# Optimization experiments

Hardware: AMD Instinct MI355X
Metric: run time of the kernel (lower is better)

## Reference

```python
import jax, jax.numpy as jnp
import numpy as np

DIM = 192
HEADS = 6
HIDDEN = 384  # int(dim * mlp_ratio)


def conv2d(x, w, b=None, padding=0, groups=1):
    out = jax.lax.conv_general_dilated(
        x, w, (1, 1), [(padding, padding), (padding, padding)],
        feature_group_count=groups,
        dimension_numbers=('NCHW', 'OIHW', 'NCHW'))
    return out if b is None else out + b[None, :, None, None]


def layernorm(x, g, b, eps=1e-5):
    m = x.mean(-1, keepdims=True)
    v = x.var(-1, keepdims=True)  # biased, matches torch LayerNorm
    return (x - m) / jnp.sqrt(v + eps) * g + b


def l2norm(x, eps=1e-12):  # F.normalize(dim=-1)
    n = jnp.linalg.norm(x, axis=-1, keepdims=True)
    return x / jnp.maximum(n, eps)


def setup_inputs() -> dict:
    key = jax.random.key(0)
    ks = jax.random.split(key, 12)
    s = 0.02
    return {
        'x': jax.random.normal(ks[0], (4, DIM, 128, 128), dtype=jnp.float32),
        'g1': jnp.ones((DIM,), jnp.float32),
        'b1': jnp.zeros((DIM,), jnp.float32),
        'w_qkv': jax.random.normal(ks[1], (3 * DIM, DIM, 1, 1), jnp.float32) * s,
        'w_dw': jax.random.normal(ks[2], (3 * DIM, 1, 3, 3), jnp.float32) * s,
        'temp': jnp.ones((HEADS, 1, 1), jnp.float32),
        'w_head': jax.random.normal(ks[3], (HEADS, HEADS, 3, 3), jnp.float32) * s,
        'w_proj': jax.random.normal(ks[4], (DIM, DIM, 1, 1), jnp.float32) * s,
        'g2': jnp.ones((DIM,), jnp.float32),
        'b2': jnp.zeros((DIM,), jnp.float32),
        'w_fc1': jax.random.normal(ks[5], (HIDDEN, DIM), jnp.float32) * s,
        'b_fc1': jnp.zeros((HIDDEN,), jnp.float32),
        'w_fc2': jax.random.normal(ks[6], (DIM, HIDDEN), jnp.float32) * s,
        'b_fc2': jnp.zeros((DIM,), jnp.float32),
        'w_sa': jax.random.normal(ks[7], (1, DIM, 3, 3), jnp.float32) * s,
        'b_sa': jnp.zeros((1,), jnp.float32),
    }


def reference(x, g1, b1, w_qkv, w_dw, temp, w_head, w_proj, g2, b2,
              w_fc1, b_fc1, w_fc2, b_fc2, w_sa, b_sa):
    b, c, h, w = x.shape
    hw = h * w
    # norm1 (note: original code re-assigns x, so residual uses normed x)
    xf = x.reshape(b, c, hw).transpose(0, 2, 1)          # [b, hw, c]
    x1 = layernorm(xf, g1, b1).transpose(0, 2, 1).reshape(b, c, h, w)
    # channel attention (Restormer style)
    qkv = conv2d(conv2d(x1, w_qkv), w_dw, padding=1, groups=3 * c)
    q, k, v = jnp.split(qkv, 3, axis=1)
    cp = c // HEADS
    q = l2norm(q.reshape(b, HEADS, cp, hw))
    k = l2norm(k.reshape(b, HEADS, cp, hw))
    v = v.reshape(b, HEADS, cp, hw)
    attn = jnp.einsum('bhcn,bhdn->bhcd', q, k) * temp    # [b, heads, cp, cp]
    attn = conv2d(attn, w_head, padding=1)               # conv over head channels
    attn = jax.nn.softmax(attn, axis=-1)
    out = jnp.einsum('bhcd,bhdn->bhcn', attn, v).reshape(b, c, h, w)
    out = conv2d(out, w_proj)
    x2 = x1 + out
    # MLP branch with spatial-gating attn
    x3 = x2.reshape(b, c, hw).transpose(0, 2, 1)         # [b, hw, c]
    y = layernorm(x3, g2, b2)
    y = jax.nn.gelu(y @ w_fc1.T + b_fc1, approximate=False)
    y = y @ w_fc2.T + b_fc2
    y = jax.nn.gelu(y, approximate=False)                # SAAttn act_fn
    y4 = y.reshape(b, h, w, c).transpose(0, 3, 1, 2)     # [b, c, h, w]
    gate = jax.nn.sigmoid(conv2d(y4, w_sa, b_sa, padding=1))  # [b,1,h,w]
    y = (y4 * gate).reshape(b, c, hw).transpose(0, 2, 1)
    x4 = x3 + y
    return x4.transpose(0, 2, 1).reshape(b, c, h, w)
```

## Files before the change

### kernel.cpp

```cpp
#include <hip/hip_runtime.h>
#include <hip/hip_bf16.h>
#include <math.h>

using bf16 = __hip_bfloat16;

static constexpr int CDIM   = 192;
static constexpr int HEADS  = 6;
static constexpr int CP     = 32;
static constexpr int HIDDEN = 384;
static constexpr int HImg   = 128;
static constexpr int WImg   = 128;
static constexpr int HW     = HImg * WImg;
static constexpr int BATCH  = 4;
static constexpr int PCHUNK = 256;
static constexpr int CSPLIT = 12;
static constexpr int DWCHUNK = 4;

typedef __attribute__((ext_vector_type(8))) short short8;
typedef __attribute__((ext_vector_type(4))) float f32x4;
typedef __attribute__((ext_vector_type(4))) unsigned short ushort4v;
typedef __attribute__((ext_vector_type(8))) unsigned short ushort8v;

template<typename T> __device__ inline float tof(T v);
template<> __device__ inline float tof<float>(float v){ return v; }
template<> __device__ inline float tof<bf16>(bf16 v){ return __bfloat162float(v); }

template<typename T> __device__ inline T fromf(float v);
template<> __device__ inline float fromf<float>(float v){ return v; }
template<> __device__ inline bf16  fromf<bf16>(float v){ return __float2bfloat16(v); }

__device__ inline unsigned short f2bf_bits(float f){
    bf16 h = __float2bfloat16(f);
    return *reinterpret_cast<unsigned short*>(&h);
}
__device__ inline float bfbits2f(unsigned short u){
    union { unsigned int i; float f; } c; c.i = ((unsigned int)u) << 16; return c.f;
}

__device__ inline float gelu_exact(float x){
    return 0.5f * x * (1.0f + erff(x * 0.70710678118654752440f));
}

__device__ inline void load4f(const float* p, float* f){
    f32x4 v = *reinterpret_cast<const f32x4*>(p);
    f[0]=v[0]; f[1]=v[1]; f[2]=v[2]; f[3]=v[3];
}
__device__ inline void load4f(const bf16* p, float* f){
    ushort4v v = *reinterpret_cast<const ushort4v*>(p);
    f[0]=bfbits2f(v[0]); f[1]=bfbits2f(v[1]); f[2]=bfbits2f(v[2]); f[3]=bfbits2f(v[3]);
}

__device__ __forceinline__ void gload16(const bf16* g, bf16* l){
    __builtin_amdgcn_global_load_lds(
        (const __attribute__((address_space(1))) void*)g,
        (__attribute__((address_space(3))) void*)l, 16, 0, 0);
}

__global__ __launch_bounds__(256) void convw_kernel(
    const float* __restrict__ w_qkv, const float* __restrict__ w_proj,
    const float* __restrict__ w_fc1, const float* __restrict__ w_fc2,
    bf16* __restrict__ wq, bf16* __restrict__ wp,
    bf16* __restrict__ wf1, bf16* __restrict__ wf2)
{
    int i = blockIdx.x * 256 + threadIdx.x;
    const int n0 = 576*192, n1 = n0 + 192*192, n2 = n1 + 384*192, n3 = n2 + 192*384;
    if (i < n0)      wq[i]       = fromf<bf16>(w_qkv[i]);
    else if (i < n1) wp[i - n0]  = fromf<bf16>(w_proj[i - n0]);
    else if (i < n2) wf1[i - n1] = fromf<bf16>(w_fc1[i - n1]);
    else if (i < n3) wf2[i - n2] = fromf<bf16>(w_fc2[i - n2]);
}

template<typename T, bool WRES>
__global__ __launch_bounds__(256) void ln_fused_kernel(
    const T* __restrict__ in, const float* __restrict__ g,
    const float* __restrict__ b, bf16* __restrict__ resF, bf16* __restrict__ outT)
{
    int z = blockIdx.y, p0 = blockIdx.x * 64;
    __shared__ float tile[CDIM][65];
    __shared__ float sred[4][64], s2red[4][64];
    __shared__ float mrow[64], rrow[64];
    const T* ib = in + (size_t)z * CDIM * HW + p0;
    int tid = threadIdx.x;
    for (int j = tid; j < CDIM * 16; j += 256){
        int c = j >> 4, p4 = (j & 15) * 4;
        float f[4];
        load4f(ib + (size_t)c * HW + p4, f);
        tile[c][p4]   = f[0]; tile[c][p4+1] = f[1];
        tile[c][p4+2] = f[2]; tile[c][p4+3] = f[3];
    }
    __syncthreads();
    int p = tid & 63, q = tid >> 6;
    float s = 0.f, s2 = 0.f;
    #pragma unroll 4
    for (int c = q * 48; c < q * 48 + 48; ++c){
        float v = tile[c][p]; s += v; s2 += v * v;
    }
    sred[q][p] = s; s2red[q][p] = s2;
    __syncthreads();
    if (tid < 64){
        float ts = sred[0][tid] + sred[1][tid] + sred[2][tid] + sred[3][tid];
        float t2 = s2red[0][tid] + s2red[1][tid] + s2red[2][tid] + s2red[3][tid];
        float mean = ts * (1.0f / CDIM);
        float var  = t2 * (1.0f / CDIM) - mean * mean;
        mrow[tid] = mean;
        rrow[tid] = rsqrtf(var + 1e-5f);
    }
    __syncthreads();
    unsigned short* oT = (unsigned short*)(outT + ((size_t)z * HW + p0) * CDIM);
    for (int j = tid; j < 64 * 48; j += 256){
        int pr = j / 48, c4 = (j % 48) * 4;
        float m = mrow[pr], r = rrow[pr];
        ushort4v o;
        #pragma unroll
        for (int k = 0; k < 4; ++k){
            int c = c4 + k;
            o[k] = f2bf_bits((tile[c][pr] - m) * r * g[c] + b[c]);
        }
        *(ushort4v*)&oT[(size_t)pr * CDIM + c4] = o;
    }
    if (WRES){
        unsigned short* oF = (unsigned short*)resF + (size_t)z * CDIM * HW + p0;
        for (int j = tid; j < CDIM * 16; j += 256){
            int c = j >> 4, p4 = (j & 15) * 4;
            float gg = g[c], bb = b[c];
            ushort4v v;
            #pragma unroll
            for (int k = 0; k < 4; ++k)
                v[k] = f2bf_bits((tile[c][p4 + k] - mrow[p4 + k]) * rrow[p4 + k] * gg + bb);
            *(ushort4v*)&oF[(size_t)c * HW + p4] = v;
        }
    }
}

template<int EPI>
__global__ __launch_bounds__(256) void gemm_mfma_kernel(
    const bf16* __restrict__ Wb, const bf16* __restrict__ XT,
    void* __restrict__ Cout, const float* __restrict__ bias,
    const bf16* __restrict__ res, int M, int K)
{
    __shared__ bf16 smem[24576];
    int z  = blockIdx.z;
    int n0 = blockIdx.x * 128;
    int m0 = blockIdx.y * 64;
    const bf16* Xb = XT + (size_t)z * (size_t)HW * K;
    int tid  = threadIdx.x;
    int lane = tid & 63, wid = tid >> 6;
    int wm = wid & 1, wn = wid >> 1;
    int r16 = lane & 15, grp = lane >> 4;

    f32x4 acc[2][4];
    #pragma unroll
    for (int i = 0; i < 2; ++i)
        #pragma unroll
        for (int j = 0; j < 4; ++j){ f32x4 zz = {0.f,0.f,0.f,0.f}; acc[i][j] = zz; }

    auto STAGE = [&](int kt, int buf){
        bf16* Al = smem + buf * 12288;
        bf16* Bl = Al + 4096;
        #pragma unroll
        for (int i = 0; i < 2; ++i){
            int s = i * 256 + tid;
            int row = s >> 3, ch = s & 7;
            gload16(Wb + (size_t)(m0 + row) * K + kt * 64 + ((ch ^ (row & 7)) * 8),
                    Al + s * 8);
        }
        #pragma unroll
        for (int i = 0; i < 4; ++i){
            int s = i * 256 + tid;
            int row = s >> 3, ch = s & 7;
            gload16(Xb + (size_t)(n0 + row) * K + kt * 64 + ((ch ^ (row & 7)) * 8),
                    Bl + s * 8);
        }
    };

    int nkt = K >> 6;
    STAGE(0, 0);
    int cur = 0;
    for (int kt = 0; kt < nkt; ++kt){
        if (kt + 1 < nkt){
            STAGE(kt + 1, cur ^ 1);
            asm volatile("s_waitcnt vmcnt(6)" ::: "memory");
        } else {
            asm volatile("s_waitcnt vmcnt(0)" ::: "memory");
        }
        __builtin_amdgcn_s_barrier();
        bf16* Al = smem + cur * 12288;
        bf16* Bl = Al + 4096;
        #pragma unroll
        for (int ks = 0; ks < 2; ++ks){
            int kel = ks * 32 + grp * 8;
            short8 a[2], b[4];
            #pragma unroll
            for (int fi = 0; fi < 2; ++fi){
                int row = wm * 32 + fi * 16 + r16;
                a[fi] = *reinterpret_cast<const short8*>(Al + row * 64 + (kel ^ ((row & 7) * 8)));
            }
            #pragma unroll
            for (int fj = 0; fj < 4; ++fj){
                int row = wn * 64 + fj * 16 + r16;
                b[fj] = *reinterpret_cast<const short8*>(Bl + row * 64 + (kel ^ ((row & 7) * 8)));
            }
            #pragma unroll
            for (int fi = 0; fi < 2; ++fi)
                #pragma unroll
                for (int fj = 0; fj < 4; ++fj)
                    acc[fi][fj] = __builtin_amdgcn_mfma_f32_16x16x32_bf16(
                        a[fi], b[fj], acc[fi][fj], 0, 0, 0);
        }
        asm volatile("s_waitcnt lgkmcnt(0)" ::: "memory");
        __builtin_amdgcn_sched_barrier(0);
        __builtin_amdgcn_s_barrier();
        cur ^= 1;
    }

    if (EPI == 3){
        unsigned short* T = (unsigned short*)smem;
        #pragma unroll
        for (int fi = 0; fi < 2; ++fi)
            #pragma unroll
            for (int fj = 0; fj < 4; ++fj){
                int nl = wn * 64 + fj * 16 + r16;
                int mb = wm * 32 + fi * 16 + grp * 4;
                #pragma unroll
                for (int rr = 0; rr < 4; ++rr){
                    float v = gelu_exact(acc[fi][fj][rr] + bias[m0 + mb + rr]);
                    T[nl * 72 + mb + rr] = f2bf_bits(v);
                }
            }
        __syncthreads();
        bf16* Y = (bf16*)Cout;
        int rrow = tid >> 1, half = tid & 1;
        const short8* srcv = reinterpret_cast<const short8*>(T + rrow * 72 + half * 32);
        short8* dstv = reinterpret_cast<short8*>(
            Y + ((size_t)z * HW + n0 + rrow) * M + m0 + half * 32);
        #pragma unroll
        for (int i = 0; i < 4; ++i) dstv[i] = srcv[i];
        return;
    }

    {
        unsigned short* T = (unsigned short*)smem;
        #pragma unroll
        for (int fi = 0; fi < 2; ++fi)
            #pragma unroll
            for (int fj = 0; fj < 4; ++fj){
                int m = wm * 32 + fi * 16 + grp * 4;
                int n = wn * 64 + fj * 16 + r16;
                #pragma unroll
                for (int rr = 0; rr < 4; ++rr)
                    T[(m + rr) * 136 + n] = f2bf_bits(acc[fi][fj][rr]);
            }
        __syncthreads();
        int row = tid >> 2, c8 = (tid & 3) * 8;
        bf16* Cb = (bf16*)Cout;
        size_t gbase = (size_t)z * M * HW + (size_t)(m0 + row) * HW + n0 + c8;
        float bv = (EPI == 2) ? bias[m0 + row] : 0.f;
        #pragma unroll
        for (int j = 0; j < 4; ++j){
            int coff = j * 32;
            ushort8v t8 = *(const ushort8v*)&T[row * 136 + c8 + coff];
            ushort8v o8;
            if (EPI == 0){
                o8 = t8;
            } else if (EPI == 1){
                ushort8v r8 = *(const ushort8v*)((const unsigned short*)res + gbase + coff);
                #pragma unroll
                for (int k = 0; k < 8; ++k)
                    o8[k] = f2bf_bits(bfbits2f(t8[k]) + bfbits2f(r8[k]));
            } else {
                #pragma unroll
                for (int k = 0; k < 8; ++k)
                    o8[k] = f2bf_bits(gelu_exact(bfbits2f(t8[k]) + bv));
            }
            *(ushort8v*)((unsigned short*)Cb + gbase + coff) = o8;
        }
    }
}

__global__ __launch_bounds__(256) void dw_kernel(
    const bf16* __restrict__ in, const float* __restrict__ wdw,
    bf16* __restrict__ out, float* __restrict__ sqp)
{
    int ch = blockIdx.y, z = blockIdx.z;
    int tid = threadIdx.x;
    int rp = tid >> 4;
    int xx = (tid & 15) * 8;
    int y0 = blockIdx.x * 32 + rp * 2;
    const unsigned short* p =
        (const unsigned short*)(in + ((size_t)z * 3 * CDIM + ch) * HW);
    float w[9];
    #pragma unroll
    for (int t = 0; t < 9; ++t) w[t] = wdw[ch * 9 + t];
    float f[4][8], lf[4], rf[4];
    #pragma unroll
    for (int r = 0; r < 4; ++r){
        int iy = y0 - 1 + r;
        if (iy >= 0 && iy < HImg){
            ushort8v v8 = *(const ushort8v*)(p + iy * WImg + xx);
            #pragma unroll
            for (int j = 0; j < 8; ++j) f[r][j] = bfbits2f(v8[j]);
        } else {
            #pragma unroll
            for (int j = 0; j < 8; ++j) f[r][j] = 0.f;
        }
        float l = __shfl_up(f[r][7], 1);
        float rr_ = __shfl_down(f[r][0], 1);
        lf[r] = (xx == 0) ? 0.f : l;
        rf[r] = (xx + 8 >= WImg) ? 0.f : rr_;
    }
    float sq = 0.f;
    unsigned short* ob = (unsigned short*)(out + ((size_t)z * 3 * CDIM + ch) * HW);
    #pragma unroll
    for (int orow = 0; orow < 2; ++orow){
        ushort8v o8;
        #pragma unroll
        for (int j = 0; j < 8; ++j){
            float a = 0.f;
            #pragma unroll
            for (int dy = 0; dy < 3; ++dy){
                int r = orow + dy;
                float e0 = (j == 0) ? lf[r] : f[r][j - 1];
                float e2 = (j == 7) ? rf[r] : f[r][j + 1];
                a = fmaf(w[dy*3], e0, fmaf(w[dy*3+1], f[r][j], fmaf(w[dy*3+2], e2, a)));
            }
            o8[j] = f2bf_bits(a);
            sq = fmaf(a, a, sq);
        }
        *(ushort8v*)(ob + (y0 + orow) * WImg + xx) = o8;
    }
    if (ch < 2 * CDIM){
        #pragma unroll
        for (int m = 1; m < 64; m <<= 1) sq += __shfl_xor(sq, m, 64);
        __shared__ float red[4];
        if ((tid & 63) == 0) red[tid >> 6] = sq;
        __syncthreads();
        if (tid == 0)
            sqp[((size_t)ch * BATCH + z) * DWCHUNK + blockIdx.x] =
                red[0] + red[1] + red[2] + red[3];
    }
}

__global__ __launch_bounds__(256) void attn_qk_kernel(
    const bf16* __restrict__ qkv, const float* __restrict__ sqp,
    const float* __restrict__ temp, float* __restrict__ part)
{
    int chunk = blockIdx.x;
    int h = blockIdx.y, z = blockIdx.z;
    __shared__ unsigned short qs[CP][PCHUNK + 4];
    __shared__ unsigned short ks[CP][PCHUNK + 4];
    __shared__ float invqs[CP], invks[CP];
    int tid = threadIdx.x;
    if (tid < 2 * CP){
        int which = tid >> 5, cc = tid & 31;
        int ch = which * CDIM + h * CP + cc;
        const float* sp = &sqp[((size_t)ch * BATCH + z) * DWCHUNK];
        float s = sp[0] + sp[1] + sp[2] + sp[3];
        float inv = 1.0f / fmaxf(sqrtf(s), 1e-12f);
        (which ? invks : invqs)[cc] = inv;
    }
    int n0 = chunk * PCHUNK;
    const unsigned short* qb = (const unsigned short*)(qkv + ((size_t)z * 3 * CDIM + h * CP) * HW);
    const unsigned short* kb = (const unsigned short*)(qkv + ((size_t)z * 3 * CDIM + CDIM + h * CP) * HW);
    for (int i = tid; i < CP * (PCHUNK / 4); i += 256){
        int r = i >> 6, p4 = i & 63;
        *(ushort4v*)&qs[r][p4 * 4] = *(const ushort4v*)&qb[(size_t)r * HW + n0 + p4 * 4];
        *(ushort4v*)&ks[r][p4 * 4] = *(const ushort4v*)&kb[(size_t)r * HW + n0 + p4 * 4];
    }
    __syncthreads();
    int c  = tid >> 3;
    int d0 = (tid & 7) * 4;
    float acc[4] = {0.f, 0.f, 0.f, 0.f};
    for (int p4 = 0; p4 < PCHUNK / 4; ++p4){
        ushort4v qv = *(const ushort4v*)&qs[c][p4 * 4];
        float qf0 = bfbits2f(qv[0]), qf1 = bfbits2f(qv[1]);
        float qf2 = bfbits2f(qv[2]), qf3 = bfbits2f(qv[3]);
        #pragma unroll
        for (int j = 0; j < 4; ++j){
            ushort4v kv = *(const ushort4v*)&ks[d0 + j][p4 * 4];
            acc[j] = fmaf(qf0, bfbits2f(kv[0]),
                     fmaf(qf1, bfbits2f(kv[1]),
                     fmaf(qf2, bfbits2f(kv[2]),
                     fmaf(qf3, bfbits2f(kv[3]), acc[j]))));
        }
    }
    float sc = invqs[c] * temp[h];
    size_t base = ((size_t)chunk * BATCH * HEADS + (size_t)z * HEADS + h) * CP * CP
                + c * CP + d0;
    #pragma unroll
    for (int j = 0; j < 4; ++j)
        part[base + j] = acc[j] * sc * invks[d0 + j];
}

__global__ __launch_bounds__(256) void attn_reduce_kernel(
    const float* __restrict__ part, float* __restrict__ attn)
{
    int idx = blockIdx.x * 256 + threadIdx.x;
    float s = 0.f;
    for (int ch = 0; ch < HW / PCHUNK; ++ch)
        s += part[(size_t)ch * (BATCH * HEADS * CP * CP) + idx];
    attn[idx] = s;
}

__global__ __launch_bounds__(256) void headconv_softmax_kernel(
    const float* __restrict__ attn, const float* __restrict__ wh,
    float* __restrict__ attn2)
{
    int oh = blockIdx.x, z = blockIdx.y;
    __shared__ float wsm[HEADS * 9];
    __shared__ float ain[HEADS][CP * CP];
    __shared__ float aout[CP * CP];
    int tid = threadIdx.x;
    if (tid < HEADS * 9) wsm[tid] = wh[oh * HEADS * 9 + tid];
    for (int i = tid; i < HEADS * CP * CP; i += 256)
        ain[i >> 10][i & 1023] = attn[((size_t)z * HEADS + (i >> 10)) * CP * CP + (i & 1023)];
    __syncthreads();
    for (int idx = tid; idx < CP * CP; idx += 256){
        int i = idx >> 5, j = idx & 31;
        float acc = 0.f;
        #pragma unroll
        for (int ih = 0; ih < HEADS; ++ih){
            #pragma unroll
            for (int dy = 0; dy < 3; ++dy){
                int ii = i + dy - 1;
                if (ii < 0 || ii >= CP) continue;
                #pragma unroll
                for (int dx = 0; dx < 3; ++dx){
                    int jj = j + dx - 1;
                    if (jj < 0 || jj >= CP) continue;
                    acc += wsm[ih * 9 + dy * 3 + dx] * ain[ih][ii * CP + jj];
                }
            }
        }
        aout[idx] = acc;
    }
    __syncthreads();
    int r = tid >> 3, l8 = tid & 7;
    float v[4];
    #pragma unroll
    for (int k = 0; k < 4; ++k) v[k] = aout[r * CP + l8 * 4 + k];
    float mx = fmaxf(fmaxf(v[0], v[1]), fmaxf(v[2], v[3]));
    #pragma unroll
    for (int m = 1; m < 8; m <<= 1) mx = fmaxf(mx, __shfl_xor(mx, m, 64));
    float sum = 0.f;
    #pragma unroll
    for (int k = 0; k < 4; ++k){ v[k] = expf(v[k] - mx); sum += v[k]; }
    #pragma unroll
    for (int m = 1; m < 8; m <<= 1) sum += __shfl_xor(sum, m, 64);
    float rs = 1.0f / sum;
    float* o = attn2 + ((size_t)z * HEADS + oh) * CP * CP + r * CP + l8 * 4;
    #pragma unroll
    for (int k = 0; k < 4; ++k) o[k] = v[k] * rs;
}

__global__ __launch_bounds__(256) void av_kernel(
    const float* __restrict__ attn2, const bf16* __restrict__ qkv, bf16* __restrict__ outT)
{
    int h = blockIdx.y, z = blockIdx.z;
    int tid = threadIdx.x;
    __shared__ float As[CP][CP];
    __shared__ unsigned short Vs[CP][PCHUNK];
    __shared__ unsigned short ot[256][36];
    for (int i = tid; i < CP * CP; i += 256)
        As[i >> 5][i & 31] = attn2[((size_t)(z * HEADS + h)) * CP * CP + i];
    int n0 = blockIdx.x * 256;
    const unsigned short* vb =
        (const unsigned short*)(qkv + ((size_t)z * 3 * CDIM + 2 * CDIM + h * CP) * HW) + n0;
    for (int i = tid; i < CP * 64; i += 256){
        int d = i >> 6, p4 = (i & 63) * 4;
        *(ushort4v*)&Vs[d][p4] = *(const ushort4v*)(vb + (size_t)d * HW + p4);
    }
    __syncthreads();
    float vreg[CP];
    #pragma unroll
    for (int d = 0; d < CP; ++d) vreg[d] = bfbits2f(Vs[d][tid]);
    for (int c = 0; c < CP; ++c){
        float acc = 0.f;
        #pragma unroll
        for (int d = 0; d < CP; ++d) acc = fmaf(As[c][d], vreg[d], acc);
        ot[tid][c] = f2bf_bits(acc);
    }
    __syncthreads();
    unsigned short* ob = (unsigned short*)outT
        + ((size_t)z * HW + (size_t)n0) * CDIM + h * CP;
    for (int j = tid; j < 256 * 8; j += 256){
        int row = j >> 3, q4 = (j & 7) * 4;
        *(ushort4v*)&ob[(size_t)row * CDIM + q4] = *(ushort4v*)&ot[row][q4];
    }
}

__global__ __launch_bounds__(256) void gate_partial_kernel(
    const bf16* __restrict__ y, const float* __restrict__ wsa,
    float* __restrict__ part_g)
{
    int cs = blockIdx.y, z = blockIdx.z;
    __shared__ float wsm[16 * 9];
    if (threadIdx.x < 144) wsm[threadIdx.x] = wsa[cs * 144 + threadIdx.x];
    __syncthreads();
    int idx = blockIdx.x * 2048 + threadIdx.x * 8;
    int yy = idx >> 7, xx = idx & 127;
    const unsigned short* yb =
        (const unsigned short*)(y + (size_t)z * CDIM * HW + (size_t)cs * 16 * HW);
    float acc[8] = {0.f,0.f,0.f,0.f,0.f,0.f,0.f,0.f};
    for (int c = 0; c < 16; ++c){
        const unsigned short* pc = yb + (size_t)c * HW;
        #pragma unroll
        for (int dy = 0; dy < 3; ++dy){
            int iy = yy + dy - 1;
            float f[8], lf, rf;
            if (iy >= 0 && iy < HImg){
                ushort8v v8 = *(const ushort8v*)(pc + iy * WImg + xx);
                #pragma unroll
                for (int j = 0; j < 8; ++j) f[j] = bfbits2f(v8[j]);
            } else {
                #pragma unroll
                for (int j = 0; j < 8; ++j) f[j] = 0.f;
            }
            float l = __shfl_up(f[7], 1);
            float r = __shfl_down(f[0], 1);
            lf = (xx == 0) ? 0.f : l;
            rf = (xx + 8 >= WImg) ? 0.f : r;
            const float* wr = &wsm[c * 9 + dy * 3];
            #pragma unroll
            for (int j = 0; j < 8; ++j){
                float e0 = (j == 0) ? lf : f[j - 1];
                float e2 = (j == 7) ? rf : f[j + 1];
                acc[j] = fmaf(wr[0], e0, fmaf(wr[1], f[j], fmaf(wr[2], e2, acc[j])));
            }
        }
    }
    float* og = &part_g[((size_t)cs * BATCH + z) * HW + idx];
    f32x4 o0 = {acc[0], acc[1], acc[2], acc[3]};
    f32x4 o1 = {acc[4], acc[5], acc[6], acc[7]};
    *(f32x4*)og = o0;
    *(f32x4*)(og + 4) = o1;
}

__global__ __launch_bounds__(256) void gate_finish_kernel(
    const float* __restrict__ part_g, const float* __restrict__ bsa,
    float* __restrict__ gate)
{
    int i4 = (blockIdx.x * 256 + threadIdx.x) * 4;
    float b0 = bsa[0];
    f32x4 acc = {b0, b0, b0, b0};
    #pragma unroll
    for (int cs = 0; cs < CSPLIT; ++cs){
        f32x4 v = *(const f32x4*)&part_g[(size_t)cs * BATCH * HW + i4];
        #pragma unroll
        for (int j = 0; j < 4; ++j) acc[j] += v[j];
    }
    f32x4 o;
    #pragma unroll
    for (int j = 0; j < 4; ++j) o[j] = 1.0f / (1.0f + expf(-acc[j]));
    *(f32x4*)&gate[i4] = o;
}

__global__ __launch_bounds__(256) void final_kernel(
    const bf16* __restrict__ x2, const bf16* __restrict__ y2,
    const float* __restrict__ gate, float* __restrict__ out)
{
    size_t i8 = ((size_t)blockIdx.x * 256 + threadIdx.x) * 8;
    int n = (int)(i8 % HW);
    int z = (int)(i8 / ((size_t)CDIM * HW));
    ushort8v a8 = *(const ushort8v*)((const unsigned short*)x2 + i8);
    ushort8v b8 = *(const ushort8v*)((const unsigned short*)y2 + i8);
    const float* gp = gate + (size_t)z * HW + n;
    f32x4 g0 = *(const f32x4*)gp;
    f32x4 g1 = *(const f32x4*)(gp + 4);
    f32x4 o0, o1;
    #pragma unroll
    for (int j = 0; j < 4; ++j){
        o0[j] = bfbits2f(a8[j])     + bfbits2f(b8[j])     * g0[j];
        o1[j] = bfbits2f(a8[j + 4]) + bfbits2f(b8[j + 4]) * g1[j];
    }
    *(f32x4*)(out + i8) = o0;
    *(f32x4*)(out + i8 + 4) = o1;
}

extern "C" void kernel_launch(void* const* d_in, const int* in_sizes, int n_in,
                              void* d_out, int out_size, void* d_ws, size_t ws_size,
                              hipStream_t stream)
{
    const float* x      = (const float*)d_in[0];
    const float* g1     = (const float*)d_in[1];
    const float* b1     = (const float*)d_in[2];
    const float* w_qkv  = (const float*)d_in[3];
    const float* w_dw   = (const float*)d_in[4];
    const float* temp   = (const float*)d_in[5];
    const float* w_head = (const float*)d_in[6];
    const float* w_proj = (const float*)d_in[7];
    const float* g2     = (const float*)d_in[8];
    const float* b2     = (const float*)d_in[9];
    const float* w_fc1  = (const float*)d_in[10];
    const float* b_fc1  = (const float*)d_in[11];
    const float* w_fc2  = (const float*)d_in[12];
    const float* b_fc2  = (const float*)d_in[13];
    const float* w_sa   = (const float*)d_in[14];
    const float* b_sa   = (const float*)d_in[15];
    float* out = (float*)d_out;

    char* ws = (char*)d_ws;
    const size_t FULL = (size_t)BATCH * CDIM * HW;

    bf16* x1 = (bf16*)ws;
    bf16* y2 = x1;
    char* R1 = ws + FULL * 2;
    bf16*  qkvA      = (bf16*)R1;
    bf16*  attn_outT = (bf16*)R1;
    bf16*  ln2T      = (bf16*)R1;
    bf16*  y1T       = (bf16*)(R1 + FULL * 2);
    char* R2 = R1 + FULL * 3 * 2;
    bf16*  x1T = (bf16*)R2;
    bf16*  dwB = (bf16*)R2;
    bf16*  x2  = (bf16*)R2;
    char* SM = R2 + FULL * 3 * 2;
    float* attn   = (float*)SM;
    float* attn2  = attn + BATCH * HEADS * CP * CP;
    float* gate   = attn2 + BATCH * HEADS * CP * CP;
    float* sqp    = gate + BATCH * HW;
    float* part   = sqp + 2 * CDIM * BATCH * DWCHUNK;
    float* part_g = part;
    bf16* wq_b  = (bf16*)(part + (HW / PCHUNK) * BATCH * HEADS * CP * CP);
    bf16* wp_b  = wq_b  + 576 * 192;
    bf16* wf1_b = wp_b  + 192 * 192;
    bf16* wf2_b = wf1_b + 384 * 192;

    dim3 blk(256);

    convw_kernel<<<dim3((294912 + 255) / 256), blk, 0, stream>>>(
        w_qkv, w_proj, w_fc1, w_fc2, wq_b, wp_b, wf1_b, wf2_b);
    ln_fused_kernel<float, true><<<dim3(HW / 64, BATCH), blk, 0, stream>>>(
        x, g1, b1, x1, x1T);
    gemm_mfma_kernel<0><<<dim3(HW / 128, (3 * CDIM) / 64, BATCH), blk, 0, stream>>>(
        wq_b, x1T, qkvA, nullptr, nullptr, 3 * CDIM, CDIM);
    dw_kernel<<<dim3(DWCHUNK, 3 * CDIM, BATCH), blk, 0, stream>>>(qkvA, w_dw, dwB, sqp);
    attn_qk_kernel<<<dim3(HW / PCHUNK, HEADS, BATCH), blk, 0, stream>>>(
        dwB, sqp, temp, part);
    attn_reduce_kernel<<<dim3((BATCH * HEADS * CP * CP) / 256), blk, 0, stream>>>(part, attn);
    headconv_softmax_kernel<<<dim3(HEADS, BATCH), blk, 0, stream>>>(attn, w_head, attn2);
    av_kernel<<<dim3(HW / 256, HEADS, BATCH), blk, 0, stream>>>(attn2, dwB, attn_outT);
    gemm_mfma_kernel<1><<<dim3(HW / 128, CDIM / 64, BATCH), blk, 0, stream>>>(
        wp_b, attn_outT, x2, nullptr, x1, CDIM, CDIM);
    ln_fused_kernel<bf16, false><<<dim3(HW / 64, BATCH), blk, 0, stream>>>(
        x2, g2, b2, nullptr, ln2T);
    gemm_mfma_kernel<3><<<dim3(HW / 128, HIDDEN / 64, BATCH), blk, 0, stream>>>(
        wf1_b, ln2T, y1T, b_fc1, nullptr, HIDDEN, CDIM);
    gemm_mfma_kernel<2><<<dim3(HW / 128, CDIM / 64, BATCH), blk, 0, stream>>>(
        wf2_b, y1T, y2, b_fc2, nullptr, CDIM, HIDDEN);
    gate_partial_kernel<<<dim3(HW / 2048, CSPLIT, BATCH), blk, 0, stream>>>(
        y2, w_sa, part_g);
    gate_finish_kernel<<<dim3(BATCH * HW / 1024), blk, 0, stream>>>(part_g, b_sa, gate);
    final_kernel<<<dim3((int)(FULL / 2048)), blk, 0, stream>>>(x2, y2, gate, out);
}
```

Before: 289.5 us.

## Single-buffer GEMM LDS staging and store gate partials in bf16

The MFMA GEMM drops its double-buffered LDS prefetch in favour of a single buffer that is loaded, waited on fully and synchronised every k-step. This halves the LDS footprint, which may allow more blocks per CU, but it gives up overlap between global loads and MFMA work. Separately, the spatial-gate partial sums are written and read as bf16 instead of fp32, halving that intermediate traffic at some cost in precision before the sigmoid.

```diff
diff --git a/kernel.cpp b/kernel.cpp
--- a/kernel.cpp
+++ b/kernel.cpp
@@ -138,7 +138,9 @@
     void* __restrict__ Cout, const float* __restrict__ bias,
     const bf16* __restrict__ res, int M, int K)
 {
-    __shared__ bf16 smem[24576];
+    __shared__ bf16 smem[12288];
+    bf16* Als = smem;
+    bf16* Bls = smem + 4096;
     int z  = blockIdx.z;
     int n0 = blockIdx.x * 128;
     int m0 = blockIdx.y * 64;
@@ -154,38 +156,24 @@
         #pragma unroll
         for (int j = 0; j < 4; ++j){ f32x4 zz = {0.f,0.f,0.f,0.f}; acc[i][j] = zz; }
 
-    auto STAGE = [&](int kt, int buf){
-        bf16* Al = smem + buf * 12288;
-        bf16* Bl = Al + 4096;
+    int nkt = K >> 6;
+    for (int kt = 0; kt < nkt; ++kt){
         #pragma unroll
         for (int i = 0; i < 2; ++i){
             int s = i * 256 + tid;
             int row = s >> 3, ch = s & 7;
             gload16(Wb + (size_t)(m0 + row) * K + kt * 64 + ((ch ^ (row & 7)) * 8),
-                    Al + s * 8);
+                    Als + s * 8);
         }
         #pragma unroll
         for (int i = 0; i < 4; ++i){
             int s = i * 256 + tid;
             int row = s >> 3, ch = s & 7;
             gload16(Xb + (size_t)(n0 + row) * K + kt * 64 + ((ch ^ (row & 7)) * 8),
-                    Bl + s * 8);
-        }
-    };
-
-    int nkt = K >> 6;
-    STAGE(0, 0);
-    int cur = 0;
-    for (int kt = 0; kt < nkt; ++kt){
-        if (kt + 1 < nkt){
-            STAGE(kt + 1, cur ^ 1);
-            asm volatile("s_waitcnt vmcnt(6)" ::: "memory");
-        } else {
-            asm volatile("s_waitcnt vmcnt(0)" ::: "memory");
-        }
-        __builtin_amdgcn_s_barrier();
-        bf16* Al = smem + cur * 12288;
-        bf16* Bl = Al + 4096;
+                    Bls + s * 8);
+        }
+        asm volatile("s_waitcnt vmcnt(0)" ::: "memory");
+        __syncthreads();
         #pragma unroll
         for (int ks = 0; ks < 2; ++ks){
             int kel = ks * 32 + grp * 8;
@@ -193,12 +181,12 @@
             #pragma unroll
             for (int fi = 0; fi < 2; ++fi){
                 int row = wm * 32 + fi * 16 + r16;
-                a[fi] = *reinterpret_cast<const short8*>(Al + row * 64 + (kel ^ ((row & 7) * 8)));
+                a[fi] = *reinterpret_cast<const short8*>(Als + row * 64 + (kel ^ ((row & 7) * 8)));
             }
             #pragma unroll
             for (int fj = 0; fj < 4; ++fj){
                 int row = wn * 64 + fj * 16 + r16;
-                b[fj] = *reinterpret_cast<const short8*>(Bl + row * 64 + (kel ^ ((row & 7) * 8)));
+                b[fj] = *reinterpret_cast<const short8*>(Bls + row * 64 + (kel ^ ((row & 7) * 8)));
             }
             #pragma unroll
             for (int fi = 0; fi < 2; ++fi)
@@ -207,10 +195,7 @@
                     acc[fi][fj] = __builtin_amdgcn_mfma_f32_16x16x32_bf16(
                         a[fi], b[fj], acc[fi][fj], 0, 0, 0);
         }
-        asm volatile("s_waitcnt lgkmcnt(0)" ::: "memory");
-        __builtin_amdgcn_sched_barrier(0);
-        __builtin_amdgcn_s_barrier();
-        cur ^= 1;
+        __syncthreads();
     }
 
     if (EPI == 3){
@@ -490,7 +475,7 @@
 
 __global__ __launch_bounds__(256) void gate_partial_kernel(
     const bf16* __restrict__ y, const float* __restrict__ wsa,
-    float* __restrict__ part_g)
+    bf16* __restrict__ part_g)
 {
     int cs = blockIdx.y, z = blockIdx.z;
     __shared__ float wsm[16 * 9];
@@ -528,15 +513,14 @@
             }
         }
     }
-    float* og = &part_g[((size_t)cs * BATCH + z) * HW + idx];
-    f32x4 o0 = {acc[0], acc[1], acc[2], acc[3]};
-    f32x4 o1 = {acc[4], acc[5], acc[6], acc[7]};
-    *(f32x4*)og = o0;
-    *(f32x4*)(og + 4) = o1;
+    ushort8v o8;
+    #pragma unroll
+    for (int j = 0; j < 8; ++j) o8[j] = f2bf_bits(acc[j]);
+    *(ushort8v*)((unsigned short*)part_g + ((size_t)cs * BATCH + z) * HW + idx) = o8;
 }
 
 __global__ __launch_bounds__(256) void gate_finish_kernel(
-    const float* __restrict__ part_g, const float* __restrict__ bsa,
+    const bf16* __restrict__ part_g, const float* __restrict__ bsa,
     float* __restrict__ gate)
 {
     int i4 = (blockIdx.x * 256 + threadIdx.x) * 4;
@@ -544,9 +528,10 @@
     f32x4 acc = {b0, b0, b0, b0};
     #pragma unroll
     for (int cs = 0; cs < CSPLIT; ++cs){
-        f32x4 v = *(const f32x4*)&part_g[(size_t)cs * BATCH * HW + i4];
-        #pragma unroll
-        for (int j = 0; j < 4; ++j) acc[j] += v[j];
+        ushort4v v = *(const ushort4v*)((const unsigned short*)part_g
+                                        + (size_t)cs * BATCH * HW + i4);
+        #pragma unroll
+        for (int j = 0; j < 4; ++j) acc[j] += bfbits2f(v[j]);
     }
     f32x4 o;
     #pragma unroll
@@ -618,7 +603,7 @@
     float* gate   = attn2 + BATCH * HEADS * CP * CP;
     float* sqp    = gate + BATCH * HW;
     float* part   = sqp + 2 * CDIM * BATCH * DWCHUNK;
-    float* part_g = part;
+    bf16*  part_g = (bf16*)part;
     bf16* wq_b  = (bf16*)(part + (HW / PCHUNK) * BATCH * HEADS * CP * CP);
     bf16* wp_b  = wq_b  + 576 * 192;
     bf16* wf1_b = wp_b  + 192 * 192;
```

After: 286.9 us. Within noise of the previous version (-0.9%).
